# Performance work log

Hardware: AMD Instinct MI355X
Metric: run time of the kernel (lower is better)

Reference implementation:

```python
import jax, jax.numpy as jnp
import numpy as np

B, DIM, IMG, HEADS, DH = 8, 512, 32, 8, 64
INNER = HEADS * DH  # == DIM, required by final reshape(b, n, c)
N = IMG * IMG
BN_EPS = 1e-5


def setup_inputs() -> dict:
    key = jax.random.key(0)
    ks = jax.random.split(key, 11)
    s = lambda k, sh: jax.random.normal(k, sh, jnp.float32) * 0.05
    return {
        "x": jax.random.normal(ks[0], (B, N, DIM), jnp.float32),
        # stacked q/k/v params, index 0=q, 1=k, 2=v
        "dw_w": s(ks[1], (3, DIM, 1, 3, 3)),   # depthwise conv kernels (OIHW, groups=DIM)
        "dw_b": s(ks[2], (3, DIM)),
        "bn_g": jnp.ones((3, DIM), jnp.float32) + s(ks[3], (3, DIM)),
        "bn_b": s(ks[4], (3, DIM)),
        "bn_m": s(ks[5], (3, DIM)),
        "bn_v": jnp.abs(jax.random.normal(ks[6], (3, DIM), jnp.float32)) + 1.0,
        "pw_w": s(ks[7], (3, INNER, DIM)),     # pointwise 1x1 conv weights
        "pw_b": s(ks[8], (3, INNER)),
        "out_w": s(ks[9], (DIM, INNER)),       # nn.Linear weight [out, in]
        "out_b": s(ks[10], (DIM,)),
    }


def _proj(x_img, dw_w, dw_b, bn_g, bn_b, bn_m, bn_v, pw_w, pw_b):
    # depthwise 3x3 conv, stride 1, pad 1
    y = jax.lax.conv_general_dilated(
        x_img, dw_w, (1, 1), [(1, 1), (1, 1)],
        dimension_numbers=("NCHW", "OIHW", "NCHW"), feature_group_count=DIM)
    y = y + dw_b[None, :, None, None]
    # eval-mode BatchNorm2d
    scale = bn_g / jnp.sqrt(bn_v + BN_EPS)
    y = (y - bn_m[None, :, None, None]) * scale[None, :, None, None] + bn_b[None, :, None, None]
    # pointwise 1x1 conv
    y = jnp.einsum("bchw,oc->bohw", y, pw_w) + pw_b[None, :, None, None]
    return y


def reference(x, dw_w, dw_b, bn_g, bn_b, bn_m, bn_v, pw_w, pw_b, out_w, out_b):
    b = x.shape[0]
    # b (l w) c -> b c l w
    xi = x.transpose(0, 2, 1).reshape(b, DIM, IMG, IMG)
    # q, k, v: b (h d) l w -> b h (l w) d
    qkv = [
        _proj(xi, dw_w[i], dw_b[i], bn_g[i], bn_b[i], bn_m[i], bn_v[i], pw_w[i], pw_b[i])
        .reshape(b, HEADS, DH, N).transpose(0, 1, 3, 2)
        for i in range(3)
    ]
    q, k, v = qkv
    att = jax.nn.softmax(jnp.einsum("bhnd,bhmd->bhnm", q, k) * (DH ** -0.5), axis=-1)
    out = jnp.einsum("bhnm,bhmd->bhnd", att, v)  # [b,h,n,d]
    out = out.transpose(0, 2, 1, 3).reshape(b, N, INNER)
    return out @ out_w.T + out_b  # to_out Linear (dropout=0)
```

## Files before the change

### kernel.cpp

```cpp
#include <hip/hip_runtime.h>
#include <hip/hip_bf16.h>

#define BB    8
#define DIMC  512
#define IMGS  32
#define NPIX  1024
#define NHEAD 8
#define DHEAD 64

typedef __attribute__((ext_vector_type(8))) short short8;
typedef __attribute__((ext_vector_type(4))) float float4v;

__device__ __forceinline__ float b2f(unsigned short u) {
  union { unsigned int i; float f; } c;
  c.i = ((unsigned int)u) << 16;
  return c.f;
}
__device__ __forceinline__ unsigned short f2b(float f) {
  union { float f; unsigned int u; } c;
  c.f = f;
  unsigned int r = c.u + 0x7fffu + ((c.u >> 16) & 1u);
  return (unsigned short)(r >> 16);
}

__device__ __forceinline__ void storeC(float* p, float v) { *p = v; }
__device__ __forceinline__ void storeC(unsigned short* p, float v) { *p = f2b(v); }

__device__ __forceinline__ void async16(const void* g, void* l) {
  __builtin_amdgcn_global_load_lds(
      (const __attribute__((address_space(1))) void*)g,
      (__attribute__((address_space(3))) void*)l, 16, 0, 0);
}

#define WAITCNT_VM0   0x0F70
#define WAITCNT_LGKM0 0xC07F

__global__ __launch_bounds__(256) void wcvt_kernel(
    const float* __restrict__ pw_w, const float* __restrict__ out_w,
    const float* __restrict__ pw_b, unsigned short* __restrict__ wbf,
    float* __restrict__ bb) {
  const int i4 = (blockIdx.x * 256 + threadIdx.x) * 4;
  float4 v = (i4 < 3 * DIMC * DIMC)
                 ? *reinterpret_cast<const float4*>(pw_w + i4)
                 : *reinterpret_cast<const float4*>(out_w + (i4 - 3 * DIMC * DIMC));
  const float sc = (i4 < DIMC * DIMC) ? 0.125f : 1.0f;
  ushort4 o;
  o.x = f2b(v.x * sc); o.y = f2b(v.y * sc); o.z = f2b(v.z * sc); o.w = f2b(v.w * sc);
  *reinterpret_cast<ushort4*>(wbf + i4) = o;
  if (blockIdx.x == 0) {
    #pragma unroll
    for (int k = 0; k < 6; ++k) {
      const int idx = threadIdx.x + k * 256;
      bb[idx] = pw_b[idx] * (idx < DIMC ? 0.125f : 1.0f);
    }
  }
}

__global__ __launch_bounds__(256) void dwbn_kernel(
    const float* __restrict__ x, const float* __restrict__ dw_w,
    const float* __restrict__ dw_b, const float* __restrict__ bn_g,
    const float* __restrict__ bn_b, const float* __restrict__ bn_m,
    const float* __restrict__ bn_v, unsigned short* __restrict__ z) {
  const int bx = blockIdx.x;
  const int b = bx >> 10, n = bx & (NPIX - 1);
  const int l = n >> 5, w = n & 31;
  const int c0 = threadIdx.x * 2;
  const float* xb = x + (size_t)b * NPIX * DIMC + c0;
  float2 xv[9];
  #pragma unroll
  for (int kh = 0; kh < 3; ++kh) {
    #pragma unroll
    for (int kw = 0; kw < 3; ++kw) {
      const int l2 = l + kh - 1, w2 = w + kw - 1;
      const bool ok = (l2 >= 0 && l2 < IMGS && w2 >= 0 && w2 < IMGS);
      xv[kh * 3 + kw] =
          ok ? *reinterpret_cast<const float2*>(xb + (size_t)(l2 * IMGS + w2) * DIMC)
             : make_float2(0.f, 0.f);
    }
  }
  #pragma unroll
  for (int i = 0; i < 3; ++i) {
    const int pc = i * DIMC + c0;
    const float* wp = dw_w + (size_t)pc * 9;
    float a0 = dw_b[pc], a1 = dw_b[pc + 1];
    #pragma unroll
    for (int k = 0; k < 9; ++k) {
      a0 = fmaf(wp[k], xv[k].x, a0);
      a1 = fmaf(wp[9 + k], xv[k].y, a1);
    }
    const float s0 = bn_g[pc] * rsqrtf(bn_v[pc] + 1e-5f);
    const float s1 = bn_g[pc + 1] * rsqrtf(bn_v[pc + 1] + 1e-5f);
    const float r0 = (a0 - bn_m[pc]) * s0 + bn_b[pc];
    const float r1 = (a1 - bn_m[pc + 1]) * s1 + bn_b[pc + 1];
    ushort2 st;
    st.x = f2b(r0);
    st.y = f2b(r1);
    *reinterpret_cast<ushort2*>(
        z + (((size_t)(i * BB + b)) * NPIX + n) * DIMC + c0) = st;
  }
}

template <typename CT>
__global__ __launch_bounds__(256) void gemm_mfma(
    const unsigned short* __restrict__ Abase,
    const unsigned short* __restrict__ Wbase,
    const float* __restrict__ biasBase, CT* __restrict__ Cbase) {
  __shared__ short As[8 * 64 * 8];
  __shared__ short Bs[8 * 64 * 8];
  const int bz = blockIdx.z;
  const int wi = bz >> 3;
  const short* A = (const short*)Abase + (size_t)bz * NPIX * DIMC;
  const short* W = (const short*)Wbase + (size_t)wi * DIMC * DIMC;
  const float* bias = biasBase + wi * DIMC;
  CT* C = Cbase + (size_t)bz * NPIX * DIMC;

  const int t = threadIdx.x;
  const int wv = t >> 6, lane = t & 63;
  const int lo = lane & 15, hi = lane >> 4;
  const int wm = wv >> 1, wn = wv & 1;
  const int m0 = blockIdx.y * 128, n0 = blockIdx.x * 128;

  float4v acc[4][4];
  #pragma unroll
  for (int i = 0; i < 4; ++i)
    #pragma unroll
    for (int j = 0; j < 4; ++j) acc[i][j] = {0.f, 0.f, 0.f, 0.f};

  for (int k0 = 0; k0 < DIMC; k0 += 32) {
    #pragma unroll
    for (int p = 0; p < 2; ++p) {
      const int sub = wv + p * 4;
      async16(A + (size_t)(m0 + sub * 16 + lo) * DIMC + k0 + hi * 8,
              As + (sub * 64 + lane) * 8);
      async16(W + (size_t)(n0 + sub * 16 + lo) * DIMC + k0 + hi * 8,
              Bs + (sub * 64 + lane) * 8);
    }
    __syncthreads();
    short8 af[4], bf[4];
    #pragma unroll
    for (int mt = 0; mt < 4; ++mt)
      af[mt] = *reinterpret_cast<const short8*>(As + ((wm * 4 + mt) * 64 + lane) * 8);
    #pragma unroll
    for (int nt = 0; nt < 4; ++nt)
      bf[nt] = *reinterpret_cast<const short8*>(Bs + ((wn * 4 + nt) * 64 + lane) * 8);
    #pragma unroll
    for (int mt = 0; mt < 4; ++mt)
      #pragma unroll
      for (int nt = 0; nt < 4; ++nt)
        acc[mt][nt] = __builtin_amdgcn_mfma_f32_16x16x32_bf16(af[mt], bf[nt],
                                                              acc[mt][nt], 0, 0, 0);
    __syncthreads();
  }

  float bv[4];
  #pragma unroll
  for (int nt = 0; nt < 4; ++nt) bv[nt] = bias[n0 + wn * 64 + nt * 16 + lo];
  #pragma unroll
  for (int mt = 0; mt < 4; ++mt) {
    #pragma unroll
    for (int r = 0; r < 4; ++r) {
      const int row = m0 + wm * 64 + mt * 16 + hi * 4 + r;
      CT* cp = C + (size_t)row * DIMC + n0 + wn * 64 + lo;
      #pragma unroll
      for (int nt = 0; nt < 4; ++nt) storeC(cp + nt * 16, acc[mt][nt][r] + bv[nt]);
    }
  }
}

__global__ __launch_bounds__(256) void vt_kernel(
    const unsigned short* __restrict__ v, unsigned short* __restrict__ vt) {
  __shared__ unsigned short tile[64][68];
  const int n0 = blockIdx.x * 64, h = blockIdx.y, b = blockIdx.z;
  const int t = threadIdx.x;
  const unsigned short* vb = v + (size_t)b * NPIX * DIMC + h * DHEAD;
  #pragma unroll
  for (int u = 0; u < 4; ++u) {
    const int lin = t + u * 256;
    const int row = lin >> 4, c4 = (lin & 15) * 4;
    *reinterpret_cast<ushort4*>(&tile[row][c4]) =
        *reinterpret_cast<const ushort4*>(vb + (size_t)(n0 + row) * DIMC + c4);
  }
  __syncthreads();
  unsigned short* vtb = vt + ((size_t)(b * NHEAD + h)) * DHEAD * NPIX;
  #pragma unroll
  for (int u = 0; u < 4; ++u) {
    const int lin = t + u * 256;
    const int d = lin >> 4, n4 = (lin & 15) * 4;
    ushort4 o;
    o.x = tile[n4 + 0][d];
    o.y = tile[n4 + 1][d];
    o.z = tile[n4 + 2][d];
    o.w = tile[n4 + 3][d];
    *reinterpret_cast<ushort4*>(vtb + (size_t)d * NPIX + n0 + n4) = o;
  }
}

__global__ __launch_bounds__(256, 2) void attn_mfma(
    const unsigned short* __restrict__ qkv, const unsigned short* __restrict__ vt,
    unsigned short* __restrict__ attn_o) {
  __shared__ char sm[53248];
  const int qt = blockIdx.x, h = blockIdx.y, b = blockIdx.z;
  const int t = threadIdx.x;
  const int wv = t >> 6, lane = t & 63;
  const int lo = lane & 15, hi = lane >> 4;

  char* wbase = sm + wv * 13312;
  short* Ks = (short*)(wbase);
  short* VTs = (short*)(wbase + 4096);
  short* Ps = (short*)(wbase + 8192);

  const short* qb = (const short*)qkv + ((size_t)(0 * BB + b) * NPIX) * DIMC + h * DHEAD;
  const short* kb = (const short*)qkv + ((size_t)(1 * BB + b) * NPIX) * DIMC + h * DHEAD;
  const short* vtb = (const short*)vt + ((size_t)(b * NHEAD + h)) * DHEAD * NPIX;

  short8 qf[4][2];
  #pragma unroll
  for (int mt = 0; mt < 4; ++mt)
    #pragma unroll
    for (int cc = 0; cc < 2; ++cc)
      qf[mt][cc] = *reinterpret_cast<const short8*>(
          qb + (size_t)(qt * 64 + mt * 16 + lo) * DIMC + cc * 32 + hi * 8);

  float4v oacc[4][4];
  float4v lsum[4];
  #pragma unroll
  for (int mt = 0; mt < 4; ++mt) {
    lsum[mt] = {0.f, 0.f, 0.f, 0.f};
    #pragma unroll
    for (int dt = 0; dt < 4; ++dt) oacc[mt][dt] = {0.f, 0.f, 0.f, 0.f};
  }

  const int n0 = wv * 256;
  for (int kt = 0; kt < 8; ++kt) {
    const int kbase = n0 + kt * 32;
    __builtin_amdgcn_s_waitcnt(WAITCNT_LGKM0);
    __builtin_amdgcn_sched_barrier(0);
    #pragma unroll
    for (int s = 0; s < 4; ++s) {
      const int nt = s >> 1, cc = s & 1;
      async16(kb + (size_t)(kbase + nt * 16 + lo) * DIMC + cc * 32 + hi * 8,
              Ks + (s * 64 + lane) * 8);
    }
    #pragma unroll
    for (int dt = 0; dt < 4; ++dt)
      async16(vtb + (size_t)(dt * 16 + lo) * NPIX + kbase + hi * 8,
              VTs + (dt * 64 + lane) * 8);
    __builtin_amdgcn_sched_barrier(0);
    __builtin_amdgcn_s_waitcnt(WAITCNT_VM0);
    __builtin_amdgcn_sched_barrier(0);

    short8 kf[2][2];
    #pragma unroll
    for (int nt = 0; nt < 2; ++nt)
      #pragma unroll
      for (int cc = 0; cc < 2; ++cc)
        kf[nt][cc] = *reinterpret_cast<const short8*>(Ks + ((nt * 2 + cc) * 64 + lane) * 8);
    float4v sacc[4][2];
    #pragma unroll
    for (int mt = 0; mt < 4; ++mt)
      #pragma unroll
      for (int nt = 0; nt < 2; ++nt) {
        sacc[mt][nt] = {0.f, 0.f, 0.f, 0.f};
        sacc[mt][nt] = __builtin_amdgcn_mfma_f32_16x16x32_bf16(qf[mt][0], kf[nt][0],
                                                               sacc[mt][nt], 0, 0, 0);
        sacc[mt][nt] = __builtin_amdgcn_mfma_f32_16x16x32_bf16(qf[mt][1], kf[nt][1],
                                                               sacc[mt][nt], 0, 0, 0);
      }

    #pragma unroll
    for (int mt = 0; mt < 4; ++mt)
      #pragma unroll
      for (int nt = 0; nt < 2; ++nt)
        #pragma unroll
        for (int r = 0; r < 4; ++r) {
          const float p = __expf(sacc[mt][nt][r]);
          Ps[(mt * 16 + hi * 4 + r) * 40 + nt * 16 + lo] = (short)f2b(p);
          lsum[mt][r] += p;
        }

    short8 vf[4];
    #pragma unroll
    for (int dt = 0; dt < 4; ++dt)
      vf[dt] = *reinterpret_cast<const short8*>(VTs + (dt * 64 + lane) * 8);
    #pragma unroll
    for (int mt = 0; mt < 4; ++mt) {
      const short8 pf = *reinterpret_cast<const short8*>(Ps + (mt * 16 + lo) * 40 + hi * 8);
      #pragma unroll
      for (int dt = 0; dt < 4; ++dt)
        oacc[mt][dt] = __builtin_amdgcn_mfma_f32_16x16x32_bf16(pf, vf[dt],
                                                               oacc[mt][dt], 0, 0, 0);
    }
  }

  #pragma unroll
  for (int mt = 0; mt < 4; ++mt)
    #pragma unroll
    for (int r = 0; r < 4; ++r) {
      float v = lsum[mt][r];
      v += __shfl_xor(v, 1);
      v += __shfl_xor(v, 2);
      v += __shfl_xor(v, 4);
      v += __shfl_xor(v, 8);
      lsum[mt][r] = v;
    }

  float* Obuf = (float*)sm;
  float* lbuf = (float*)(sm + 16384);
  float* linv = (float*)(sm + 17408);
  __syncthreads();
  if (lo == 0) {
    #pragma unroll
    for (int mt = 0; mt < 4; ++mt)
      #pragma unroll
      for (int r = 0; r < 4; ++r) lbuf[wv * 64 + mt * 16 + hi * 4 + r] = lsum[mt][r];
  }
  __syncthreads();
  if (t < 64) linv[t] = 1.0f / (lbuf[t] + lbuf[64 + t] + lbuf[128 + t] + lbuf[192 + t]);

  unsigned short* aob = attn_o + ((size_t)b * NPIX + qt * 64) * DIMC + h * DHEAD;
  #pragma unroll
  for (int mt = 0; mt < 4; ++mt) {
    __syncthreads();
    #pragma unroll
    for (int dt = 0; dt < 4; ++dt)
      #pragma unroll
      for (int r = 0; r < 4; ++r)
        Obuf[wv * 1024 + (dt * 4 + r) * 64 + lane] = oacc[mt][dt][r];
    __syncthreads();
    #pragma unroll
    for (int k2 = 0; k2 < 4; ++k2) {
      const int e = t + k2 * 256;
      const float sum2 = Obuf[e] + Obuf[1024 + e] + Obuf[2048 + e] + Obuf[3072 + e];
      const int dt = e >> 8, r = (e >> 6) & 3, le = e & 63;
      const int row = mt * 16 + (le >> 4) * 4 + r, d = dt * 16 + (le & 15);
      aob[(size_t)row * DIMC + d] = f2b(sum2 * linv[row]);
    }
  }
}

extern "C" void kernel_launch(void* const* d_in, const int* in_sizes, int n_in,
                              void* d_out, int out_size, void* d_ws, size_t ws_size,
                              hipStream_t stream) {
  const float* x    = (const float*)d_in[0];
  const float* dw_w = (const float*)d_in[1];
  const float* dw_b = (const float*)d_in[2];
  const float* bn_g = (const float*)d_in[3];
  const float* bn_b = (const float*)d_in[4];
  const float* bn_m = (const float*)d_in[5];
  const float* bn_v = (const float*)d_in[6];
  const float* pw_w = (const float*)d_in[7];
  const float* pw_b = (const float*)d_in[8];
  const float* out_w = (const float*)d_in[9];
  const float* out_b = (const float*)d_in[10];
  float* out = (float*)d_out;

  unsigned short* z   = (unsigned short*)d_ws;
  unsigned short* qkv = z + (size_t)3 * BB * NPIX * DIMC;
  unsigned short* wbf = qkv + (size_t)3 * BB * NPIX * DIMC;
  float* bb = (float*)(wbf + (size_t)4 * DIMC * DIMC);
  unsigned short* vtb = z;
  unsigned short* attn_o = z + (size_t)BB * NHEAD * DHEAD * NPIX;

  wcvt_kernel<<<dim3(1024), 256, 0, stream>>>(pw_w, out_w, pw_b, wbf, bb);
  dwbn_kernel<<<dim3(BB * NPIX), 256, 0, stream>>>(x, dw_w, dw_b, bn_g, bn_b,
                                                   bn_m, bn_v, z);
  gemm_mfma<unsigned short><<<dim3(4, 8, 24), 256, 0, stream>>>(z, wbf, bb, qkv);
  vt_kernel<<<dim3(16, NHEAD, BB), 256, 0, stream>>>(
      qkv + (size_t)2 * BB * NPIX * DIMC, vtb);
  attn_mfma<<<dim3(16, NHEAD, BB), 256, 0, stream>>>(qkv, vtb, attn_o);
  gemm_mfma<float><<<dim3(4, 8, 8), 256, 0, stream>>>(
      attn_o, wbf + (size_t)3 * DIMC * DIMC, out_b, out);
}
```

Baseline: 230.1 us.

## Fold BN into depthwise weights and tile dwconv over rows for window reuse

Precomputes BN-scaled, channel-transposed depthwise weights and a fused shift in the weight-conversion kernel, so the depthwise kernel no longer recomputes BN and gathers strided weights per pixel. The depthwise kernel now handles 4 output rows by 2 columns per block, with 4 channels per thread, and keeps a 6x3 register window so input loads are reused across rows. The cost is more registers per thread and far fewer blocks.

```diff
diff --git a/kernel.cpp b/kernel.cpp
--- a/kernel.cpp
+++ b/kernel.cpp
@@ -37,8 +37,12 @@
 
 __global__ __launch_bounds__(256) void wcvt_kernel(
     const float* __restrict__ pw_w, const float* __restrict__ out_w,
-    const float* __restrict__ pw_b, unsigned short* __restrict__ wbf,
-    float* __restrict__ bb) {
+    const float* __restrict__ pw_b, const float* __restrict__ dw_w,
+    const float* __restrict__ dw_b, const float* __restrict__ bn_g,
+    const float* __restrict__ bn_b, const float* __restrict__ bn_m,
+    const float* __restrict__ bn_v, unsigned short* __restrict__ wbf,
+    float* __restrict__ bb, float* __restrict__ wT,
+    float* __restrict__ shiftv) {
   const int i4 = (blockIdx.x * 256 + threadIdx.x) * 4;
   float4 v = (i4 < 3 * DIMC * DIMC)
                  ? *reinterpret_cast<const float4*>(pw_w + i4)
@@ -47,56 +51,79 @@
   ushort4 o;
   o.x = f2b(v.x * sc); o.y = f2b(v.y * sc); o.z = f2b(v.z * sc); o.w = f2b(v.w * sc);
   *reinterpret_cast<ushort4*>(wbf + i4) = o;
-  if (blockIdx.x == 0) {
-    #pragma unroll
-    for (int k = 0; k < 6; ++k) {
-      const int idx = threadIdx.x + k * 256;
-      bb[idx] = pw_b[idx] * (idx < DIMC ? 0.125f : 1.0f);
+  const int idx = blockIdx.x * 256 + threadIdx.x;
+  if (idx < 6 * 256) {
+    if (idx < 3 * DIMC / 2) {
+      #pragma unroll
+      for (int hh = 0; hh < 2; ++hh) {
+        const int id2 = idx * 2 + hh;
+        const int i = id2 >> 9, c = id2 & 511;
+        const float scale = bn_g[id2] * rsqrtf(bn_v[id2] + 1e-5f);
+        shiftv[id2] = (dw_b[id2] - bn_m[id2]) * scale + bn_b[id2];
+        #pragma unroll
+        for (int t = 0; t < 9; ++t)
+          wT[(i * 9 + t) * DIMC + c] = dw_w[(size_t)id2 * 9 + t] * scale;
+      }
+    }
+    #pragma unroll
+    for (int k = 0; k < 1; ++k) {
+      if (idx < 3 * DIMC)
+        bb[idx] = pw_b[idx] * (idx < DIMC ? 0.125f : 1.0f);
     }
   }
 }
 
 __global__ __launch_bounds__(256) void dwbn_kernel(
-    const float* __restrict__ x, const float* __restrict__ dw_w,
-    const float* __restrict__ dw_b, const float* __restrict__ bn_g,
-    const float* __restrict__ bn_b, const float* __restrict__ bn_m,
-    const float* __restrict__ bn_v, unsigned short* __restrict__ z) {
-  const int bx = blockIdx.x;
-  const int b = bx >> 10, n = bx & (NPIX - 1);
-  const int l = n >> 5, w = n & 31;
-  const int c0 = threadIdx.x * 2;
-  const float* xb = x + (size_t)b * NPIX * DIMC + c0;
-  float2 xv[9];
-  #pragma unroll
-  for (int kh = 0; kh < 3; ++kh) {
-    #pragma unroll
-    for (int kw = 0; kw < 3; ++kw) {
-      const int l2 = l + kh - 1, w2 = w + kw - 1;
-      const bool ok = (l2 >= 0 && l2 < IMGS && w2 >= 0 && w2 < IMGS);
-      xv[kh * 3 + kw] =
-          ok ? *reinterpret_cast<const float2*>(xb + (size_t)(l2 * IMGS + w2) * DIMC)
-             : make_float2(0.f, 0.f);
-    }
-  }
+    const float* __restrict__ x, const float* __restrict__ wT,
+    const float* __restrict__ shiftv, unsigned short* __restrict__ z) {
+  const int wp = blockIdx.x, lg = blockIdx.y, b = blockIdx.z;
+  const int t = threadIdx.x;
+  const int c = (t & 127) * 4;
+  const int w = wp * 2 + (t >> 7);
+  const int l0 = lg * 4;
+  const float* xb = x + (size_t)b * NPIX * DIMC + c;
+
+  const float4 zero4 = make_float4(0.f, 0.f, 0.f, 0.f);
+  float4 win[6][3];
+  #pragma unroll
+  for (int rr = 0; rr < 6; ++rr) {
+    const int l = l0 - 1 + rr;
+    #pragma unroll
+    for (int dw = 0; dw < 3; ++dw) {
+      const int ww = w - 1 + dw;
+      const bool ok = ((unsigned)l < IMGS) && ((unsigned)ww < IMGS);
+      win[rr][dw] = ok ? *reinterpret_cast<const float4*>(
+                             xb + (size_t)(l * IMGS + ww) * DIMC)
+                       : zero4;
+    }
+  }
+
   #pragma unroll
   for (int i = 0; i < 3; ++i) {
-    const int pc = i * DIMC + c0;
-    const float* wp = dw_w + (size_t)pc * 9;
-    float a0 = dw_b[pc], a1 = dw_b[pc + 1];
-    #pragma unroll
-    for (int k = 0; k < 9; ++k) {
-      a0 = fmaf(wp[k], xv[k].x, a0);
-      a1 = fmaf(wp[9 + k], xv[k].y, a1);
-    }
-    const float s0 = bn_g[pc] * rsqrtf(bn_v[pc] + 1e-5f);
-    const float s1 = bn_g[pc + 1] * rsqrtf(bn_v[pc + 1] + 1e-5f);
-    const float r0 = (a0 - bn_m[pc]) * s0 + bn_b[pc];
-    const float r1 = (a1 - bn_m[pc + 1]) * s1 + bn_b[pc + 1];
-    ushort2 st;
-    st.x = f2b(r0);
-    st.y = f2b(r1);
-    *reinterpret_cast<ushort2*>(
-        z + (((size_t)(i * BB + b)) * NPIX + n) * DIMC + c0) = st;
+    float4 wv[9];
+    #pragma unroll
+    for (int tp = 0; tp < 9; ++tp)
+      wv[tp] = *reinterpret_cast<const float4*>(wT + (i * 9 + tp) * DIMC + c);
+    const float4 sh = *reinterpret_cast<const float4*>(shiftv + i * DIMC + c);
+    #pragma unroll
+    for (int r = 0; r < 4; ++r) {
+      float a0 = sh.x, a1 = sh.y, a2 = sh.z, a3 = sh.w;
+      #pragma unroll
+      for (int kh = 0; kh < 3; ++kh)
+        #pragma unroll
+        for (int kw = 0; kw < 3; ++kw) {
+          const float4 wq = wv[kh * 3 + kw];
+          const float4 xq = win[r + kh][kw];
+          a0 = fmaf(wq.x, xq.x, a0);
+          a1 = fmaf(wq.y, xq.y, a1);
+          a2 = fmaf(wq.z, xq.z, a2);
+          a3 = fmaf(wq.w, xq.w, a3);
+        }
+      ushort4 st;
+      st.x = f2b(a0); st.y = f2b(a1); st.z = f2b(a2); st.w = f2b(a3);
+      *reinterpret_cast<ushort4*>(
+          z + (((size_t)(i * BB + b)) * NPIX + (l0 + r) * IMGS + w) * DIMC + c) = st;
+    }
   }
 }
 
@@ -358,12 +385,15 @@
   unsigned short* qkv = z + (size_t)3 * BB * NPIX * DIMC;
   unsigned short* wbf = qkv + (size_t)3 * BB * NPIX * DIMC;
   float* bb = (float*)(wbf + (size_t)4 * DIMC * DIMC);
+  float* wT = bb + 3 * DIMC;
+  float* shiftv = wT + 3 * 9 * DIMC;
   unsigned short* vtb = z;
   unsigned short* attn_o = z + (size_t)BB * NHEAD * DHEAD * NPIX;
 
-  wcvt_kernel<<<dim3(1024), 256, 0, stream>>>(pw_w, out_w, pw_b, wbf, bb);
-  dwbn_kernel<<<dim3(BB * NPIX), 256, 0, stream>>>(x, dw_w, dw_b, bn_g, bn_b,
-                                                   bn_m, bn_v, z);
+  wcvt_kernel<<<dim3(1024), 256, 0, stream>>>(pw_w, out_w, pw_b, dw_w, dw_b,
+                                              bn_g, bn_b, bn_m, bn_v, wbf, bb,
+                                              wT, shiftv);
+  dwbn_kernel<<<dim3(16, 8, BB), 256, 0, stream>>>(x, wT, shiftv, z);
   gemm_mfma<unsigned short><<<dim3(4, 8, 24), 256, 0, stream>>>(z, wbf, bb, qkv);
   vt_kernel<<<dim3(16, NHEAD, BB), 256, 0, stream>>>(
       qkv + (size_t)2 * BB * NPIX * DIMC, vtb);
```

Measured after the change: 204.2 us. -11.3%, faster.
